# Kernel tuning notes

Hardware: AMD Instinct MI355X
Metric: run time of the kernel (lower is better)

The kernel has to match this reference:

```python
import jax, jax.numpy as jnp
import numpy as np

E = 8
D_IN = 1024
D_HID = 4096
D_OUT = 1024
N_TOK = 32768  # total tokens; equal split of 4096 per expert


def setup_inputs() -> dict:
    key = jax.random.key(0)
    k_in, k_w1, k_w2 = jax.random.split(key, 3)
    inputs = jax.random.normal(k_in, (N_TOK, D_IN), dtype=jnp.float32)
    expert_size = jnp.full((E,), N_TOK // E, dtype=jnp.int64)
    # reset_parameters: normal(0, 1/sqrt(fan_in)) per expert
    w1 = jax.random.normal(k_w1, (E, D_IN, D_HID), dtype=jnp.float32) / np.sqrt(D_IN)
    b1 = jnp.zeros((E, D_HID), dtype=jnp.float32)
    w2 = jax.random.normal(k_w2, (E, D_HID, D_OUT), dtype=jnp.float32) / np.sqrt(D_HID)
    b2 = jnp.zeros((E, D_OUT), dtype=jnp.float32)
    return {"inputs": inputs, "expert_size": expert_size,
            "w1": w1, "b1": b1, "w2": w2, "b2": b2}


def reference(inputs, expert_size, w1, b1, w2, b2):
    # Grouped GEMM over contiguous per-expert splits. expert_size is equal
    # per expert (N_TOK // E), so the variable-split loop in the torch code
    # collapses to a batched einsum with identical math.
    e = w1.shape[0]
    n, d = inputs.shape
    cap = n // e  # tokens per expert (equal splits)
    x = inputs.reshape(e, cap, d)                       # [E, cap, D_IN]
    h = jnp.einsum('ecd,edh->ech', x, w1) + b1[:, None, :]
    h = jax.nn.gelu(h, approximate=False)               # F.gelu default = erf gelu
    y = jnp.einsum('ech,eho->eco', h, w2) + b2[:, None, :]
    return y.reshape(n, -1)                             # [N_TOK, D_OUT]
```

## Files before the change

### kernel.cpp

```cpp
#include <hip/hip_runtime.h>
#include <hip/hip_bf16.h>
#include <type_traits>

#define NE 8
#define DIN 1024
#define DHID 4096
#define DOUTD 1024
#define NTOK 32768
#define CAP (NTOK / NE)

typedef unsigned short u16;
typedef __attribute__((ext_vector_type(8))) short bf16x8;
typedef __attribute__((ext_vector_type(4))) float f32x4;

template <int I> using ic = std::integral_constant<int, I>;

__device__ __forceinline__ u16 f2bf(float x) {
  unsigned u = __builtin_bit_cast(unsigned, x);
  u += 0x7fffu + ((u >> 16) & 1u);
  return (u16)(u >> 16);
}

__device__ __forceinline__ float gelu_f(float x) {
  float u = 0.7978845608028654f * x * (1.0f + 0.044715f * x * x);
  float t = __expf(-2.0f * fabsf(u));
  float r = __fdividef(2.0f * t, 1.0f + t);
  float th = copysignf(1.0f - r, u);
  return 0.5f * x * (1.0f + th);
}

__device__ __forceinline__ void async_ld16(const void* g, void* l) {
  __builtin_amdgcn_global_load_lds(
      (const __attribute__((address_space(1))) unsigned int*)g,
      (__attribute__((address_space(3))) unsigned int*)l, 16, 0, 0);
}

__global__ __launch_bounds__(256) void convert_bf16_kernel(const float* __restrict__ in,
                                                           u16* __restrict__ out) {
  size_t i = ((size_t)blockIdx.x * 256 + threadIdx.x) * 8;
  float4 a = *(const float4*)(in + i);
  float4 b = *(const float4*)(in + i + 4);
  uint4 o;
  o.x = (unsigned)f2bf(a.x) | ((unsigned)f2bf(a.y) << 16);
  o.y = (unsigned)f2bf(a.z) | ((unsigned)f2bf(a.w) << 16);
  o.z = (unsigned)f2bf(b.x) | ((unsigned)f2bf(b.y) << 16);
  o.w = (unsigned)f2bf(b.z) | ((unsigned)f2bf(b.w) << 16);
  *(uint4*)(out + i) = o;
}

__global__ __launch_bounds__(256) void transpose_bf16_kernel(const float* __restrict__ in,
                                                             u16* __restrict__ out,
                                                             int K, int N) {
  __shared__ __align__(16) u16 tile[64 * 72];
  const int e = blockIdx.z;
  const int n0 = blockIdx.x * 64;
  const int k0 = blockIdx.y * 64;
  const float* inp = in + (size_t)e * K * N;
  u16* outp = out + (size_t)e * N * K;
  const int t = threadIdx.x;
  const int kr = t >> 4;
  const int nc = (t & 15) * 4;
#pragma unroll
  for (int rr = 0; rr < 4; ++rr) {
    int kl = rr * 16 + kr;
    float4 v = *(const float4*)(inp + (size_t)(k0 + kl) * N + n0 + nc);
    tile[(nc + 0) * 72 + kl] = f2bf(v.x);
    tile[(nc + 1) * 72 + kl] = f2bf(v.y);
    tile[(nc + 2) * 72 + kl] = f2bf(v.z);
    tile[(nc + 3) * 72 + kl] = f2bf(v.w);
  }
  __syncthreads();
  const int nr = t >> 3;
  const int kc = (t & 7) * 8;
#pragma unroll
  for (int it = 0; it < 2; ++it) {
    int nl = it * 32 + nr;
    bf16x8 w = *(const bf16x8*)(tile + nl * 72 + kc);
    *(bf16x8*)(outp + (size_t)(n0 + nl) * K + k0 + kc) = w;
  }
}

template <int K, int N, bool GELU_OUT>
__global__ __launch_bounds__(512, 2) void moe_gemm256_kernel(
    const u16* __restrict__ A, const u16* __restrict__ Bt,
    const float* __restrict__ bias, void* __restrict__ Out) {
  extern __shared__ __align__(16) char smem_raw[];
  constexpr int TX = N / 256;
  constexpr int NT = K / 32;
  static_assert(NT % 2 == 0 && NT >= 4, "K-tile count");
  static_assert(TX == 4 || TX == 16, "supertile map assumes TX in {4,16}");

  const int bid = blockIdx.x;
  const int e = bid & 7;
  const int idx = bid >> 3;
  constexpr int STC = TX / 4;
  const int st = idx >> 4;
  const int win = idx & 15;
  const int m0 = ((st / STC) * 4 + (win >> 2)) * 256;
  const int n0 = ((st % STC) * 4 + (win & 3)) * 256;

  const u16* Ae = A + (size_t)e * CAP * K;
  const u16* Be = Bt + (size_t)e * N * K;

  const int tid = threadIdx.x;
  const int l = tid & 63;
  const int w = tid >> 6;
  const int wr = w >> 2;
  const int wc = w & 3;
  const int g = l >> 4;
  const int rl = l & 15;

  int aoff[8], boff[4];
#pragma unroll
  for (int j = 0; j < 8; ++j) {
    int r = wr * 128 + j * 16 + rl;
    int r7 = r & 127;
    int lu = (r >> 7) * 4 + g;
    aoff[j] = r7 * 128 + ((lu ^ (r7 & 7)) << 4);
  }
#pragma unroll
  for (int i = 0; i < 4; ++i) {
    int r = wc * 64 + i * 16 + rl;
    int r7 = r & 127;
    int lu = (r >> 7) * 4 + g;
    boff[i] = 16384 + r7 * 128 + ((lu ^ (r7 & 7)) << 4);
  }

  auto mkoff = [&](int sidx, int base0) -> size_t {
    int lrow = sidx >> 3, pu = sidx & 7;
    int lu = pu ^ (lrow & 7);
    int r = lrow + ((lu & 4) << 5);
    return (size_t)(base0 + r) * K + (lu & 3) * 8;
  };
  const u16* gA0 = Ae + mkoff(tid, m0);
  const u16* gA1 = Ae + mkoff(512 + tid, m0);
  const u16* gB0 = Be + mkoff(tid, n0);
  const u16* gB1 = Be + mkoff(512 + tid, n0);
  const int dA0 = tid * 16, dA1 = 8192 + tid * 16;
  const int dB0 = 16384 + tid * 16, dB1 = 24576 + tid * 16;

  f32x4 acc[8][4] = {};

  async_ld16((const char*)gA0, smem_raw + dA0);
  async_ld16((const char*)gA1, smem_raw + dA1);
  async_ld16((const char*)gB0, smem_raw + dB0);
  async_ld16((const char*)gB1, smem_raw + dB1);
  asm volatile("s_waitcnt vmcnt(0)\n\ts_barrier" ::: "memory");
  __builtin_amdgcn_sched_barrier(0);

  auto tileb = [&](auto JC, auto STc, auto GATEc) {
    constexpr int J = decltype(JC)::value;
    constexpr bool ST = decltype(STc)::value;
    constexpr bool GATE = decltype(GATEc)::value;
    constexpr int KOFF = (J + 1) * 64;
    const char* sr = smem_raw + J * 32768;
    char* sd = (char*)smem_raw + (J ^ 1) * 32768;
    if constexpr (ST) {
      async_ld16((const char*)gA0 + KOFF, sd + dA0);
      async_ld16((const char*)gA1 + KOFF, sd + dA1);
      async_ld16((const char*)gB0 + KOFF, sd + dB0);
      async_ld16((const char*)gB1 + KOFF, sd + dB1);
    }
    bf16x8 bfr[4], afr[8];
#pragma unroll
    for (int i = 0; i < 4; ++i) bfr[i] = *(const bf16x8*)(sr + boff[i]);
#pragma unroll
    for (int j = 0; j < 8; ++j) afr[j] = *(const bf16x8*)(sr + aoff[j]);
    asm volatile("s_waitcnt lgkmcnt(0)" ::: "memory");
    __builtin_amdgcn_sched_barrier(0);
    __builtin_amdgcn_s_setprio(1);
#pragma unroll
    for (int j = 0; j < 8; ++j)
#pragma unroll
      for (int i = 0; i < 4; ++i)
        acc[j][i] = __builtin_amdgcn_mfma_f32_16x16x32_bf16(bfr[i], afr[j], acc[j][i], 0, 0, 0);
    __builtin_amdgcn_s_setprio(0);
    if constexpr (GATE) {
      asm volatile("s_waitcnt vmcnt(0)\n\ts_barrier" ::: "memory");
      __builtin_amdgcn_sched_barrier(0);
    }
  };

#pragma unroll 1
  for (int gq = 0; gq < NT / 2 - 1; ++gq) {
    tileb(ic<0>{}, std::true_type{}, std::true_type{});
    tileb(ic<1>{}, std::true_type{}, std::true_type{});
    gA0 += 64; gA1 += 64; gB0 += 64; gB1 += 64;
  }
  tileb(ic<0>{}, std::true_type{}, std::true_type{});
  tileb(ic<1>{}, std::false_type{}, std::false_type{});

  const float* be = bias + (size_t)e * N;
  const int mb = m0 + wr * 128 + rl;
  const int nb = n0 + wc * 64 + g * 4;
  if constexpr (GELU_OUT) {
    u16* Oe = (u16*)Out + (size_t)e * (size_t)CAP * N;
#pragma unroll
    for (int j = 0; j < 8; ++j) {
      int m = mb + j * 16;
#pragma unroll
      for (int i = 0; i < 4; ++i) {
        int n = nb + i * 16;
        float4 bv = *(const float4*)(be + n);
        ushort4 o;
        o.x = f2bf(gelu_f(acc[j][i][0] + bv.x));
        o.y = f2bf(gelu_f(acc[j][i][1] + bv.y));
        o.z = f2bf(gelu_f(acc[j][i][2] + bv.z));
        o.w = f2bf(gelu_f(acc[j][i][3] + bv.w));
        *(ushort4*)(Oe + (size_t)m * N + n) = o;
      }
    }
  } else {
    float* Oe = (float*)Out + (size_t)e * (size_t)CAP * N;
#pragma unroll
    for (int j = 0; j < 8; ++j) {
      int m = mb + j * 16;
#pragma unroll
      for (int i = 0; i < 4; ++i) {
        int n = nb + i * 16;
        float4 bv = *(const float4*)(be + n);
        float4 o;
        o.x = acc[j][i][0] + bv.x;
        o.y = acc[j][i][1] + bv.y;
        o.z = acc[j][i][2] + bv.z;
        o.w = acc[j][i][3] + bv.w;
        *(float4*)(Oe + (size_t)m * N + n) = o;
      }
    }
  }
}

extern "C" void kernel_launch(void* const* d_in, const int* in_sizes, int n_in,
                              void* d_out, int out_size, void* d_ws, size_t ws_size,
                              hipStream_t stream) {
  const float* x  = (const float*)d_in[0];
  const float* w1 = (const float*)d_in[2];
  const float* b1 = (const float*)d_in[3];
  const float* w2 = (const float*)d_in[4];
  const float* b2 = (const float*)d_in[5];
  float* out = (float*)d_out;

  char* wsp = (char*)d_ws;
  u16* x_bf = (u16*)(wsp);
  u16* w1t  = (u16*)(wsp + (size_t)67108864);
  u16* w2t  = (u16*)(wsp + (size_t)134217728);
  u16* h    = (u16*)(wsp + (size_t)201326592);

  convert_bf16_kernel<<<(NTOK * DIN) / (256 * 8), 256, 0, stream>>>(x, x_bf);
  transpose_bf16_kernel<<<dim3(DHID / 64, DIN / 64, NE), 256, 0, stream>>>(w1, w1t, DIN, DHID);
  transpose_bf16_kernel<<<dim3(DOUTD / 64, DHID / 64, NE), 256, 0, stream>>>(w2, w2t, DHID, DOUTD);

  moe_gemm256_kernel<DIN, DHID, true>
      <<<dim3(NE * (CAP / 256) * (DHID / 256)), 512, 65536, stream>>>(x_bf, w1t, b1, h);
  moe_gemm256_kernel<DHID, DOUTD, false>
      <<<dim3(NE * (CAP / 256) * (DOUTD / 256)), 512, 65536, stream>>>(h, w2t, b2, out);
}
```

Measured before the change: 755.8 us.

## Deepen GEMM K-step to 64 with phased A/B loads and 128KB LDS

```diff
diff --git a/kernel.cpp b/kernel.cpp
--- a/kernel.cpp
+++ b/kernel.cpp
@@ -86,7 +86,7 @@
     const float* __restrict__ bias, void* __restrict__ Out) {
   extern __shared__ __align__(16) char smem_raw[];
   constexpr int TX = N / 256;
-  constexpr int NT = K / 32;
+  constexpr int NT = K / 64;
   static_assert(NT % 2 == 0 && NT >= 4, "K-tile count");
   static_assert(TX == 4 || TX == 16, "supertile map assumes TX in {4,16}");
 
@@ -123,7 +123,7 @@
     int r = wc * 64 + i * 16 + rl;
     int r7 = r & 127;
     int lu = (r >> 7) * 4 + g;
-    boff[i] = 16384 + r7 * 128 + ((lu ^ (r7 & 7)) << 4);
+    boff[i] = r7 * 128 + ((lu ^ (r7 & 7)) << 4);
   }
 
   auto mkoff = [&](int sidx, int base0) -> size_t {
@@ -136,59 +136,85 @@
   const u16* gA1 = Ae + mkoff(512 + tid, m0);
   const u16* gB0 = Be + mkoff(tid, n0);
   const u16* gB1 = Be + mkoff(512 + tid, n0);
-  const int dA0 = tid * 16, dA1 = 8192 + tid * 16;
-  const int dB0 = 16384 + tid * 16, dB1 = 24576 + tid * 16;
+  const int dL0 = tid * 16;
+  const int dL1 = 8192 + tid * 16;
 
   f32x4 acc[8][4] = {};
-
-  async_ld16((const char*)gA0, smem_raw + dA0);
-  async_ld16((const char*)gA1, smem_raw + dA1);
-  async_ld16((const char*)gB0, smem_raw + dB0);
-  async_ld16((const char*)gB1, smem_raw + dB1);
-  asm volatile("s_waitcnt vmcnt(0)\n\ts_barrier" ::: "memory");
-  __builtin_amdgcn_sched_barrier(0);
-
-  auto tileb = [&](auto JC, auto STc, auto GATEc) {
-    constexpr int J = decltype(JC)::value;
-    constexpr bool ST = decltype(STc)::value;
-    constexpr bool GATE = decltype(GATEc)::value;
-    constexpr int KOFF = (J + 1) * 64;
-    const char* sr = smem_raw + J * 32768;
-    char* sd = (char*)smem_raw + (J ^ 1) * 32768;
-    if constexpr (ST) {
-      async_ld16((const char*)gA0 + KOFF, sd + dA0);
-      async_ld16((const char*)gA1 + KOFF, sd + dA1);
-      async_ld16((const char*)gB0 + KOFF, sd + dB0);
-      async_ld16((const char*)gB1 + KOFF, sd + dB1);
-    }
-    bf16x8 bfr[4], afr[8];
-#pragma unroll
-    for (int i = 0; i < 4; ++i) bfr[i] = *(const bf16x8*)(sr + boff[i]);
-#pragma unroll
-    for (int j = 0; j < 8; ++j) afr[j] = *(const bf16x8*)(sr + aoff[j]);
+  bf16x8 bfr[4];
+
+  auto phase = [&](auto KCc, auto MHc, auto SWc, auto GNc,
+                   const char* bufr, char* bufs, const int stE) {
+    constexpr int KC = decltype(KCc)::value;
+    constexpr int MH = decltype(MHc)::value;
+    constexpr int SW = decltype(SWc)::value;
+    constexpr int GN = decltype(GNc)::value;
+    if constexpr (SW == 0) {
+      async_ld16(gA0 + stE + KC * 32, bufs + KC * 16384 + dL0);
+      async_ld16(gA1 + stE + KC * 32, bufs + KC * 16384 + dL1);
+    } else if constexpr (SW == 1) {
+      async_ld16(gB0 + stE + KC * 32, bufs + 32768 + KC * 16384 + dL0);
+      async_ld16(gB1 + stE + KC * 32, bufs + 32768 + KC * 16384 + dL1);
+    }
+    const char* ra = bufr + KC * 16384;
+    const char* rb = bufr + 32768 + KC * 16384;
+    bf16x8 afr[4];
+    if constexpr (MH == 0) {
+#pragma unroll
+      for (int i = 0; i < 4; ++i) bfr[i] = *(const bf16x8*)(rb + boff[i]);
+    }
+#pragma unroll
+    for (int j = 0; j < 4; ++j) afr[j] = *(const bf16x8*)(ra + aoff[MH * 4 + j]);
+    if constexpr (GN >= 0) {
+      asm volatile("s_waitcnt vmcnt(%0)\n\ts_barrier" :: "n"(GN) : "memory");
+    } else {
+      __builtin_amdgcn_s_barrier();
+    }
     asm volatile("s_waitcnt lgkmcnt(0)" ::: "memory");
     __builtin_amdgcn_sched_barrier(0);
     __builtin_amdgcn_s_setprio(1);
 #pragma unroll
-    for (int j = 0; j < 8; ++j)
+    for (int j = 0; j < 4; ++j)
 #pragma unroll
       for (int i = 0; i < 4; ++i)
-        acc[j][i] = __builtin_amdgcn_mfma_f32_16x16x32_bf16(bfr[i], afr[j], acc[j][i], 0, 0, 0);
+        acc[MH * 4 + j][i] = __builtin_amdgcn_mfma_f32_16x16x32_bf16(
+            bfr[i], afr[j], acc[MH * 4 + j][i], 0, 0, 0);
     __builtin_amdgcn_s_setprio(0);
-    if constexpr (GATE) {
-      asm volatile("s_waitcnt vmcnt(0)\n\ts_barrier" ::: "memory");
-      __builtin_amdgcn_sched_barrier(0);
-    }
   };
 
+  auto tile = [&](auto Jc, auto STc, auto LASTc) {
+    constexpr int J = decltype(Jc)::value;
+    constexpr bool STg = decltype(STc)::value;
+    constexpr bool LAST = decltype(LASTc)::value;
+    const char* bufr = smem_raw + J * 65536;
+    char* bufs = (char*)smem_raw + (J ^ 1) * 65536;
+    constexpr int SA = STg ? 0 : 2;
+    constexpr int SB = STg ? 1 : 2;
+    const int stE = (J + 1) * 64;
+    phase(ic<0>{}, ic<0>{}, ic<SA>{}, ic<-1>{}, bufr, bufs, stE);
+    phase(ic<0>{}, ic<1>{}, ic<SB>{}, ic<(LAST ? 0 : 4)>{}, bufr, bufs, stE);
+    phase(ic<1>{}, ic<0>{}, ic<SA>{}, ic<-1>{}, bufr, bufs, stE);
+    phase(ic<1>{}, ic<1>{}, ic<SB>{}, ic<(LAST ? -1 : 4)>{}, bufr, bufs, stE);
+  };
+
+  async_ld16(gA0, smem_raw + dL0);
+  async_ld16(gA1, smem_raw + dL1);
+  async_ld16(gB0, smem_raw + 32768 + dL0);
+  async_ld16(gB1, smem_raw + 32768 + dL1);
+  async_ld16(gA0 + 32, smem_raw + 16384 + dL0);
+  async_ld16(gA1 + 32, smem_raw + 16384 + dL1);
+  async_ld16(gB0 + 32, smem_raw + 49152 + dL0);
+  async_ld16(gB1 + 32, smem_raw + 49152 + dL1);
+  asm volatile("s_waitcnt vmcnt(4)\n\ts_barrier" ::: "memory");
+  __builtin_amdgcn_sched_barrier(0);
+
 #pragma unroll 1
-  for (int gq = 0; gq < NT / 2 - 1; ++gq) {
-    tileb(ic<0>{}, std::true_type{}, std::true_type{});
-    tileb(ic<1>{}, std::true_type{}, std::true_type{});
-    gA0 += 64; gA1 += 64; gB0 += 64; gB1 += 64;
-  }
-  tileb(ic<0>{}, std::true_type{}, std::true_type{});
-  tileb(ic<1>{}, std::false_type{}, std::false_type{});
+  for (int pr = 0; pr < NT / 2 - 1; ++pr) {
+    tile(ic<0>{}, std::true_type{}, std::false_type{});
+    tile(ic<1>{}, std::true_type{}, std::false_type{});
+    gA0 += 128; gA1 += 128; gB0 += 128; gB1 += 128;
+  }
+  tile(ic<0>{}, std::true_type{}, std::false_type{});
+  tile(ic<1>{}, std::false_type{}, std::true_type{});
 
   const float* be = bias + (size_t)e * N;
   const int mb = m0 + wr * 128 + rl;
@@ -246,12 +272,17 @@
   u16* w2t  = (u16*)(wsp + (size_t)134217728);
   u16* h    = (u16*)(wsp + (size_t)201326592);
 
+  hipFuncSetAttribute(reinterpret_cast<const void*>(moe_gemm256_kernel<DIN, DHID, true>),
+                      hipFuncAttributeMaxDynamicSharedMemorySize, 131072);
+  hipFuncSetAttribute(reinterpret_cast<const void*>(moe_gemm256_kernel<DHID, DOUTD, false>),
+                      hipFuncAttributeMaxDynamicSharedMemorySize, 131072);
+
   convert_bf16_kernel<<<(NTOK * DIN) / (256 * 8), 256, 0, stream>>>(x, x_bf);
   transpose_bf16_kernel<<<dim3(DHID / 64, DIN / 64, NE), 256, 0, stream>>>(w1, w1t, DIN, DHID);
   transpose_bf16_kernel<<<dim3(DOUTD / 64, DHID / 64, NE), 256, 0, stream>>>(w2, w2t, DHID, DOUTD);
 
   moe_gemm256_kernel<DIN, DHID, true>
-      <<<dim3(NE * (CAP / 256) * (DHID / 256)), 512, 65536, stream>>>(x_bf, w1t, b1, h);
+      <<<dim3(NE * (CAP / 256) * (DHID / 256)), 512, 131072, stream>>>(x_bf, w1t, b1, h);
   moe_gemm256_kernel<DHID, DOUTD, false>
-      <<<dim3(NE * (CAP / 256) * (DOUTD / 256)), 512, 65536, stream>>>(h, w2t, b2, out);
-}
+      <<<dim3(NE * (CAP / 256) * (DOUTD / 256)), 512, 131072, stream>>>(h, w2t, b2, out);
+}
```

After: 718.1 us (median of 3 runs). 5.0% less time.

## Switch grouped GEMM from 256x256x32 to 128x128x64 tiles with split LDS waits

Applied to the files above, without the earlier changes.

```diff
diff --git a/kernel.cpp b/kernel.cpp
--- a/kernel.cpp
+++ b/kernel.cpp
@@ -81,23 +81,23 @@
 }
 
 template <int K, int N, bool GELU_OUT>
-__global__ __launch_bounds__(512, 2) void moe_gemm256_kernel(
+__global__ __launch_bounds__(256, 2) void moe_gemm128_kernel(
     const u16* __restrict__ A, const u16* __restrict__ Bt,
     const float* __restrict__ bias, void* __restrict__ Out) {
   extern __shared__ __align__(16) char smem_raw[];
-  constexpr int TX = N / 256;
-  constexpr int NT = K / 32;
+  constexpr int TX = N / 128;
+  constexpr int NT = K / 64;
   static_assert(NT % 2 == 0 && NT >= 4, "K-tile count");
-  static_assert(TX == 4 || TX == 16, "supertile map assumes TX in {4,16}");
+  static_assert(TX % 8 == 0, "supertile map needs TX%8==0");
 
   const int bid = blockIdx.x;
   const int e = bid & 7;
   const int idx = bid >> 3;
-  constexpr int STC = TX / 4;
-  const int st = idx >> 4;
-  const int win = idx & 15;
-  const int m0 = ((st / STC) * 4 + (win >> 2)) * 256;
-  const int n0 = ((st % STC) * 4 + (win & 3)) * 256;
+  constexpr int STC = TX / 8;
+  const int st = idx >> 6;
+  const int win = idx & 63;
+  const int m0 = ((st / STC) * 8 + (win >> 3)) * 128;
+  const int n0 = ((st % STC) * 8 + (win & 7)) * 128;
 
   const u16* Ae = A + (size_t)e * CAP * K;
   const u16* Be = Bt + (size_t)e * N * K;
@@ -105,98 +105,109 @@
   const int tid = threadIdx.x;
   const int l = tid & 63;
   const int w = tid >> 6;
-  const int wr = w >> 2;
-  const int wc = w & 3;
+  const int wr = w >> 1;
+  const int wc = w & 1;
   const int g = l >> 4;
   const int rl = l & 15;
 
-  int aoff[8], boff[4];
-#pragma unroll
-  for (int j = 0; j < 8; ++j) {
-    int r = wr * 128 + j * 16 + rl;
-    int r7 = r & 127;
-    int lu = (r >> 7) * 4 + g;
-    aoff[j] = r7 * 128 + ((lu ^ (r7 & 7)) << 4);
+  int aoff0[4], aoff1[4], boff0[4], boff1[4];
+#pragma unroll
+  for (int j = 0; j < 4; ++j) {
+    int r = wr * 64 + j * 16 + rl;
+    aoff0[j] = r * 128 + (((0 * 4 + g) ^ (r & 7)) << 4);
+    aoff1[j] = r * 128 + (((1 * 4 + g) ^ (r & 7)) << 4);
   }
 #pragma unroll
   for (int i = 0; i < 4; ++i) {
     int r = wc * 64 + i * 16 + rl;
-    int r7 = r & 127;
-    int lu = (r >> 7) * 4 + g;
-    boff[i] = 16384 + r7 * 128 + ((lu ^ (r7 & 7)) << 4);
-  }
-
-  auto mkoff = [&](int sidx, int base0) -> size_t {
-    int lrow = sidx >> 3, pu = sidx & 7;
+    boff0[i] = 16384 + r * 128 + (((0 * 4 + g) ^ (r & 7)) << 4);
+    boff1[i] = 16384 + r * 128 + (((1 * 4 + g) ^ (r & 7)) << 4);
+  }
+
+  auto mkoff = [&](int s, int base0) -> size_t {
+    int lrow = s >> 3, pu = s & 7;
     int lu = pu ^ (lrow & 7);
-    int r = lrow + ((lu & 4) << 5);
-    return (size_t)(base0 + r) * K + (lu & 3) * 8;
+    return (size_t)(base0 + lrow) * K + lu * 8;
   };
-  const u16* gA0 = Ae + mkoff(tid, m0);
-  const u16* gA1 = Ae + mkoff(512 + tid, m0);
-  const u16* gB0 = Be + mkoff(tid, n0);
-  const u16* gB1 = Be + mkoff(512 + tid, n0);
-  const int dA0 = tid * 16, dA1 = 8192 + tid * 16;
-  const int dB0 = 16384 + tid * 16, dB1 = 24576 + tid * 16;
-
-  f32x4 acc[8][4] = {};
-
-  async_ld16((const char*)gA0, smem_raw + dA0);
-  async_ld16((const char*)gA1, smem_raw + dA1);
-  async_ld16((const char*)gB0, smem_raw + dB0);
-  async_ld16((const char*)gB1, smem_raw + dB1);
+  const u16* pA[4];
+  const u16* pB[4];
+#pragma unroll
+  for (int r = 0; r < 4; ++r) {
+    pA[r] = Ae + mkoff(r * 256 + tid, m0);
+    pB[r] = Be + mkoff(r * 256 + tid, n0);
+  }
+  const int dsl = tid * 16;
+
+  f32x4 acc[4][4] = {};
+
+#pragma unroll
+  for (int r = 0; r < 4; ++r) async_ld16(pA[r], smem_raw + r * 4096 + dsl);
+#pragma unroll
+  for (int r = 0; r < 4; ++r) async_ld16(pB[r], smem_raw + 16384 + r * 4096 + dsl);
   asm volatile("s_waitcnt vmcnt(0)\n\ts_barrier" ::: "memory");
   __builtin_amdgcn_sched_barrier(0);
 
-  auto tileb = [&](auto JC, auto STc, auto GATEc) {
-    constexpr int J = decltype(JC)::value;
-    constexpr bool ST = decltype(STc)::value;
-    constexpr bool GATE = decltype(GATEc)::value;
-    constexpr int KOFF = (J + 1) * 64;
-    const char* sr = smem_raw + J * 32768;
-    char* sd = (char*)smem_raw + (J ^ 1) * 32768;
-    if constexpr (ST) {
-      async_ld16((const char*)gA0 + KOFF, sd + dA0);
-      async_ld16((const char*)gA1 + KOFF, sd + dA1);
-      async_ld16((const char*)gB0 + KOFF, sd + dB0);
-      async_ld16((const char*)gB1 + KOFF, sd + dB1);
-    }
-    bf16x8 bfr[4], afr[8];
-#pragma unroll
-    for (int i = 0; i < 4; ++i) bfr[i] = *(const bf16x8*)(sr + boff[i]);
-#pragma unroll
-    for (int j = 0; j < 8; ++j) afr[j] = *(const bf16x8*)(sr + aoff[j]);
+  auto tile = [&](auto Jc, auto STc, auto LASTc) {
+    constexpr int J = decltype(Jc)::value;
+    constexpr bool STg = decltype(STc)::value;
+    constexpr bool LAST = decltype(LASTc)::value;
+    const char* bufr = smem_raw + J * 32768;
+    char* bufs = (char*)smem_raw + (J ^ 1) * 32768;
+    const int stE = (J + 1) * 64;
+    if constexpr (STg) {
+#pragma unroll
+      for (int r = 0; r < 4; ++r) async_ld16(pA[r] + stE, bufs + r * 4096 + dsl);
+#pragma unroll
+      for (int r = 0; r < 4; ++r) async_ld16(pB[r] + stE, bufs + 16384 + r * 4096 + dsl);
+    }
+    bf16x8 b0[4], a0[4], b1[4], a1[4];
+#pragma unroll
+    for (int i = 0; i < 4; ++i) b0[i] = *(const bf16x8*)(bufr + boff0[i]);
+#pragma unroll
+    for (int j = 0; j < 4; ++j) a0[j] = *(const bf16x8*)(bufr + aoff0[j]);
+#pragma unroll
+    for (int i = 0; i < 4; ++i) b1[i] = *(const bf16x8*)(bufr + boff1[i]);
+#pragma unroll
+    for (int j = 0; j < 4; ++j) a1[j] = *(const bf16x8*)(bufr + aoff1[j]);
+    asm volatile("s_waitcnt lgkmcnt(8)" ::: "memory");
+    __builtin_amdgcn_sched_barrier(0);
+    __builtin_amdgcn_s_setprio(1);
+#pragma unroll
+    for (int j = 0; j < 4; ++j)
+#pragma unroll
+      for (int i = 0; i < 4; ++i)
+        acc[j][i] = __builtin_amdgcn_mfma_f32_16x16x32_bf16(b0[i], a0[j], acc[j][i], 0, 0, 0);
     asm volatile("s_waitcnt lgkmcnt(0)" ::: "memory");
     __builtin_amdgcn_sched_barrier(0);
-    __builtin_amdgcn_s_setprio(1);
-#pragma unroll
-    for (int j = 0; j < 8; ++j)
+#pragma unroll
+    for (int j = 0; j < 4; ++j)
 #pragma unroll
       for (int i = 0; i < 4; ++i)
-        acc[j][i] = __builtin_amdgcn_mfma_f32_16x16x32_bf16(bfr[i], afr[j], acc[j][i], 0, 0, 0);
+        acc[j][i] = __builtin_amdgcn_mfma_f32_16x16x32_bf16(b1[i], a1[j], acc[j][i], 0, 0, 0);
     __builtin_amdgcn_s_setprio(0);
-    if constexpr (GATE) {
+    if constexpr (!LAST) {
       asm volatile("s_waitcnt vmcnt(0)\n\ts_barrier" ::: "memory");
       __builtin_amdgcn_sched_barrier(0);
     }
   };
 
 #pragma unroll 1
-  for (int gq = 0; gq < NT / 2 - 1; ++gq) {
-    tileb(ic<0>{}, std::true_type{}, std::true_type{});
-    tileb(ic<1>{}, std::true_type{}, std::true_type{});
-    gA0 += 64; gA1 += 64; gB0 += 64; gB1 += 64;
-  }
-  tileb(ic<0>{}, std::true_type{}, std::true_type{});
-  tileb(ic<1>{}, std::false_type{}, std::false_type{});
+  for (int pr = 0; pr < NT / 2 - 1; ++pr) {
+    tile(ic<0>{}, std::true_type{}, std::false_type{});
+    tile(ic<1>{}, std::true_type{}, std::false_type{});
+#pragma unroll
+    for (int r = 0; r < 4; ++r) { pA[r] += 128; pB[r] += 128; }
+  }
+  tile(ic<0>{}, std::true_type{}, std::false_type{});
+  tile(ic<1>{}, std::false_type{}, std::true_type{});
 
   const float* be = bias + (size_t)e * N;
-  const int mb = m0 + wr * 128 + rl;
+  const int mb = m0 + wr * 64 + rl;
   const int nb = n0 + wc * 64 + g * 4;
   if constexpr (GELU_OUT) {
     u16* Oe = (u16*)Out + (size_t)e * (size_t)CAP * N;
 #pragma unroll
-    for (int j = 0; j < 8; ++j) {
+    for (int j = 0; j < 4; ++j) {
       int m = mb + j * 16;
 #pragma unroll
       for (int i = 0; i < 4; ++i) {
@@ -213,7 +224,7 @@
   } else {
     float* Oe = (float*)Out + (size_t)e * (size_t)CAP * N;
 #pragma unroll
-    for (int j = 0; j < 8; ++j) {
+    for (int j = 0; j < 4; ++j) {
       int m = mb + j * 16;
 #pragma unroll
       for (int i = 0; i < 4; ++i) {
@@ -246,12 +257,17 @@
   u16* w2t  = (u16*)(wsp + (size_t)134217728);
   u16* h    = (u16*)(wsp + (size_t)201326592);
 
+  hipFuncSetAttribute(reinterpret_cast<const void*>(moe_gemm128_kernel<DIN, DHID, true>),
+                      hipFuncAttributeMaxDynamicSharedMemorySize, 65536);
+  hipFuncSetAttribute(reinterpret_cast<const void*>(moe_gemm128_kernel<DHID, DOUTD, false>),
+                      hipFuncAttributeMaxDynamicSharedMemorySize, 65536);
+
   convert_bf16_kernel<<<(NTOK * DIN) / (256 * 8), 256, 0, stream>>>(x, x_bf);
   transpose_bf16_kernel<<<dim3(DHID / 64, DIN / 64, NE), 256, 0, stream>>>(w1, w1t, DIN, DHID);
   transpose_bf16_kernel<<<dim3(DOUTD / 64, DHID / 64, NE), 256, 0, stream>>>(w2, w2t, DHID, DOUTD);
 
-  moe_gemm256_kernel<DIN, DHID, true>
-      <<<dim3(NE * (CAP / 256) * (DHID / 256)), 512, 65536, stream>>>(x_bf, w1t, b1, h);
-  moe_gemm256_kernel<DHID, DOUTD, false>
-      <<<dim3(NE * (CAP / 256) * (DOUTD / 256)), 512, 65536, stream>>>(h, w2t, b2, out);
-}
+  moe_gemm128_kernel<DIN, DHID, true>
+      <<<dim3(NE * (CAP / 128) * (DHID / 128)), 256, 65536, stream>>>(x_bf, w1t, b1, h);
+  moe_gemm128_kernel<DHID, DOUTD, false>
+      <<<dim3(NE * (CAP / 128) * (DOUTD / 128)), 256, 65536, stream>>>(h, w2t, b2, out);
+}
```

After: 784.0 us. 3.7% more time.
